# Kernel tuning notes

Measured on AMD Instinct MI355X. Metric: run time of the kernel, lower is better.

Reference implementation:

```python
import jax, jax.numpy as jnp
import numpy as np
from jax import lax

KERNEL = 3      # patch size
STRIDE = 1      # matching stride at low res
RATE = 2        # downsample rate
SOFTMAX_SCALE = 10.0


def _extract_patches(img, k, stride):
    """tf.image.extract_patches with SAME padding. img: [B,H,W,C] -> [B, oh*ow, k, k, C]."""
    B, H, W, C = img.shape
    oh = -(-H // stride)
    ow = -(-W // stride)
    ph = max((oh - 1) * stride + k - H, 0)
    pw = max((ow - 1) * stride + k - W, 0)
    img = jnp.pad(img, ((0, 0), (ph // 2, ph - ph // 2), (pw // 2, pw - pw // 2), (0, 0)))
    # stack the k*k shifted strided views; channel-last order matches TF's (kh, kw, C) flattening
    cols = [img[:, dh:dh + (oh - 1) * stride + 1:stride, dw:dw + (ow - 1) * stride + 1:stride, :]
            for dh in range(k) for dw in range(k)]
    p = jnp.stack(cols, axis=3)  # [B, oh, ow, k*k, C]
    return p.reshape(B, oh * ow, k, k, C)


def _avgpool2(x):
    """Exact equivalent of TF bilinear (antialias=False) downsample by factor 2."""
    B, H, W, C = x.shape
    return x.reshape(B, H // 2, 2, W // 2, 2, C).mean(axis=(2, 4))


def _conv_same(x4, w):
    return lax.conv_general_dilated(x4, w, (1, 1), 'SAME',
                                    dimension_numbers=('NHWC', 'HWIO', 'NHWC'))


def _forward(x, mask):
    B, H, W, C = x.shape
    k, stride, rate = KERNEL, STRIDE, RATE
    h, w = H // rate, W // rate
    L = h * w

    # raw (full-res) patches used for reconstruction: [B,k,k,C,L]
    raw_w = jnp.transpose(_extract_patches(x, k, rate * stride), (0, 2, 3, 4, 1))
    # low-res foreground / background (identical here, as in the source)
    f = _avgpool2(x)              # [B,h,w,C]
    m = _avgpool2(mask)           # [B,h,w,1]
    # low-res matching patches: [B,k,k,C,L]
    wp = jnp.transpose(_extract_patches(f, k, stride), (0, 2, 3, 4, 1))
    # mask patches -> gate: mm = 1 where the 3x3 mask patch mean is exactly 1.0
    mp = _extract_patches(m, k, stride)                       # [B,L,k,k,1]
    mm = (jnp.mean(mp, axis=(2, 3, 4)) == 1.0).astype(jnp.float32)  # [B,L]

    fuse_w = jnp.eye(KERNEL, dtype=jnp.float32).reshape(KERNEL, KERNEL, 1, 1)

    def per_item(xi, wi, rwi, mmi):
        # xi:[h,w,C]  wi,rwi:[k,k,C,L]  mmi:[L]
        wn = wi / jnp.maximum(jnp.sqrt(jnp.sum(wi * wi, axis=(0, 1, 2))), 1e-4)
        yi = _conv_same(xi[None], wn)          # [1,h,w,L] cosine-similarity logits
        att = yi[0]
        # fuse: diagonal conv over the [L,L] score matrix in both patch orderings
        z = yi.reshape(1, L, L, 1)
        z = _conv_same(z, fuse_w)
        z = z.reshape(1, h, w, h, w).transpose(0, 2, 1, 4, 3).reshape(1, L, L, 1)
        z = _conv_same(z, fuse_w)
        z = z.reshape(1, w, h, w, h).transpose(0, 2, 1, 4, 3)
        yi = z.reshape(1, h, w, L)
        mm4 = mmi.reshape(1, 1, 1, L)
        yi = jax.nn.softmax(yi * mm4 * SOFTMAX_SCALE, axis=3) * mm4
        # reconstruction: transposed conv with raw full-res patches as filters
        out = lax.conv_transpose(yi, rwi, (rate, rate), 'SAME',
                                 dimension_numbers=('NHWC', 'HWIO', 'NHWC'),
                                 transpose_kernel=True) / float(rate * rate)
        return out[0], att

    y, att = jax.vmap(per_item)(f, wp, raw_w, mm)
    return y, att


def setup_inputs() -> dict:
    key = jax.random.key(0)
    x = jax.random.normal(key, (2, 128, 128, 64), dtype=jnp.float32)
    # binary hole mask: ones inside a centered 64x64 square
    mask = jnp.zeros((2, 128, 128, 1), jnp.float32).at[:, 32:96, 32:96, :].set(1.0)
    return {"x": x, "mask": mask}


def reference(x, mask):
    return _forward(x, mask)
```

## Files before the change

### kernel.cpp

```cpp
#include <hip/hip_runtime.h>
#include <hip/hip_bf16.h>

typedef _Float16 f16x8 __attribute__((ext_vector_type(8)));
typedef float f32x4 __attribute__((ext_vector_type(4)));

__device__ __forceinline__ void gload_lds16(const void* gptr, void* lptr) {
  __builtin_amdgcn_global_load_lds(
      (const __attribute__((address_space(1))) void*)gptr,
      (__attribute__((address_space(3))) void*)lptr, 16, 0, 0);
}

__global__ __launch_bounds__(256) void k_pre(const float* __restrict__ x,
                                             const float* __restrict__ mask,
                                             _Float16* __restrict__ f_h,
                                             float* __restrict__ sumsq,
                                             float* __restrict__ mlow) {
  int wave = threadIdx.x >> 6, c = threadIdx.x & 63;
  int blk = blockIdx.x * 4 + wave;
  int b = blk >> 12, ij = blk & 4095;
  int i = ij >> 6, j = ij & 63;
  size_t base = ((size_t)(b * 128 + 2 * i) * 128 + 2 * j) * 64 + c;
  float f = 0.25f * (x[base] + x[base + 64] + x[base + 128 * 64] + x[base + 128 * 64 + 64]);
  f_h[(size_t)blk * 64 + c] = (_Float16)f;
  float fsq = f * f;
  for (int off = 32; off; off >>= 1) fsq += __shfl_down(fsq, off);
  if (c == 0) {
    sumsq[blk] = fsq;
    size_t mb = (size_t)(b * 128 + 2 * i) * 128 + 2 * j;
    mlow[blk] = 0.25f * (mask[mb] + mask[mb + 1] + mask[mb + 128] + mask[mb + 129]);
  }
}

__global__ void k_norm_mm(const float* __restrict__ sumsq, const float* __restrict__ mlow,
                          float* __restrict__ invn, float* __restrict__ mmb) {
  int t = blockIdx.x * 256 + threadIdx.x;
  int b = t >> 12, l = t & 4095;
  int li = l >> 6, lj = l & 63;
  float s = 0.f;
  bool ok = true;
  for (int dh = -1; dh <= 1; ++dh)
    for (int dw = -1; dw <= 1; ++dw) {
      int ii = li + dh, jj = lj + dw;
      float mv = 0.f;
      if ((unsigned)ii < 64u && (unsigned)jj < 64u) {
        int idx = (b << 12) + ii * 64 + jj;
        s += sumsq[idx];
        mv = mlow[idx];
      }
      ok = ok && (mv == 1.0f);
    }
  invn[t] = 1.0f / fmaxf(sqrtf(s), 1e-4f);
  mmb[t] = ok ? 1.0f : 0.0f;
}

__global__ __launch_bounds__(1024) void k_compact(const float* __restrict__ mmb,
                                                  int* __restrict__ actIdx,
                                                  int* __restrict__ nAct) {
  int b = blockIdx.x;
  int t = threadIdx.x;
  int lane = t & 63, wv = t >> 6;
  __shared__ int wsum[16];
  __shared__ int sbase;
  if (t == 0) sbase = 0;
  __syncthreads();
  for (int chunk = 0; chunk < 4; ++chunk) {
    int l = chunk * 1024 + t;
    int flag = (mmb[(b << 12) + l] == 1.0f) ? 1 : 0;
    unsigned long long m = __ballot(flag);
    int wpre = __popcll(m & ((1ull << lane) - 1ull));
    if (lane == 0) wsum[wv] = __popcll(m);
    __syncthreads();
    int off = sbase;
    for (int w2 = 0; w2 < wv; ++w2) off += wsum[w2];
    if (flag) {
      int pos = off + wpre;
      if (pos < 1024) actIdx[(b << 10) + pos] = l;
    }
    __syncthreads();
    if (t == 0) {
      int s2 = 0;
      for (int w2 = 0; w2 < 16; ++w2) s2 += wsum[w2];
      sbase += s2;
    }
    __syncthreads();
  }
  int total = sbase;
  if (t >= total) actIdx[(b << 10) + t] = 0;
  if (t == 0) nAct[b] = (total > 1024) ? 1024 : total;
}

__global__ __launch_bounds__(256) void k_build_p(const _Float16* __restrict__ f_h,
                                                 _Float16* __restrict__ P) {
  int wave = threadIdx.x >> 6, c = threadIdx.x & 63;
  int blk = blockIdx.x * 4 + wave;
  int b = blk >> 12, l = blk & 4095;
  int li = l >> 6, lj = l & 63;
  _Float16* dst = P + (size_t)blk * 576 + c;
#pragma unroll
  for (int kk = 0; kk < 9; ++kk) {
    int kh = kk / 3, kw = kk % 3;
    int ii = li + kh - 1, jj = lj + kw - 1;
    _Float16 v = (_Float16)0.f;
    if ((unsigned)ii < 64u && (unsigned)jj < 64u)
      v = f_h[((size_t)(b << 12) + ii * 64 + jj) * 64 + c];
    dst[kk * 64] = v;
  }
}

__global__ void k_build_rt(const float* __restrict__ x, _Float16* __restrict__ Rt) {
  int kh = blockIdx.x, li = blockIdx.y, b = blockIdx.z;
  int r = 2 * li + kh;
  __shared__ float xrow[128 * 65];
  if (r < 128) {
    for (int t = threadIdx.x; t < 8192; t += 256) {
      int v = t >> 6, c = t & 63;
      xrow[v * 65 + c] = x[((size_t)(b * 128 + r) * 128 + v) * 64 + c];
    }
  }
  __syncthreads();
  for (int idx = threadIdx.x; idx < 12288; idx += 256) {
    int lj = idx & 63, rest = idx >> 6;
    int c = rest & 63, kw = rest >> 6;
    int v = 2 * lj + kw;
    float val = (r < 128 && v < 128) ? xrow[v * 65 + c] : 0.f;
    int n = (kh * 3 + kw) * 64 + c;
    Rt[((size_t)b * 640 + n) * 4096 + li * 64 + lj] = (_Float16)val;
  }
}

__global__ void k_rtsub(const _Float16* __restrict__ Rt, const int* __restrict__ actIdx,
                        _Float16* __restrict__ Rts) {
  int n = blockIdx.x, b = blockIdx.y;
  const _Float16* src = Rt + ((size_t)b * 640 + n) * 4096;
  _Float16* dst = Rts + ((size_t)b * 640 + n) * 1024;
  const int* aIdx = actIdx + (b << 10);
  for (int s = threadIdx.x; s < 1024; s += 256) dst[s] = src[aIdx[s]];
}

__global__ __launch_bounds__(256) void k_gemm_sim(const _Float16* __restrict__ P,
                                                  const float* __restrict__ invn,
                                                  float* __restrict__ att) {
  int b = blockIdx.z;
  const _Float16* Ab = P + (size_t)b * 4096 * 576;
  int idx = blockIdx.x;
  int bj = (int)((sqrtf(8.f * (float)idx + 1.f) - 1.f) * 0.5f);
  while ((bj + 1) * (bj + 2) / 2 <= idx) ++bj;
  while (bj * (bj + 1) / 2 > idx) --bj;
  int bi = idx - bj * (bj + 1) / 2;
  int rowBase = bi * 128, colBase = bj * 128;
  bool diag = (bi == bj);

  __shared__ alignas(16) _Float16 As[128 * 32];
  __shared__ alignas(16) _Float16 Bs[128 * 32];
  __shared__ alignas(16) float tbuf[32][132];
  int tid = threadIdx.x, wave = tid >> 6, lane = tid & 63;
  int q = lane >> 4, rr = lane & 15;
  int wr = (wave >> 1) * 64, wc = (wave & 1) * 64;
  f32x4 acc[4][4] = {};
  for (int kt = 0; kt < 576; kt += 32) {
    __syncthreads();
#pragma unroll
    for (int t = 0; t < 2; ++t) {
      int chunk = t * 256 + wave * 64 + lane;
      int row = chunk >> 2, kc = (chunk & 3) * 8;
      gload_lds16(Ab + (size_t)(rowBase + row) * 576 + kt + kc,
                  As + (size_t)(t * 256 + wave * 64) * 8);
      if (!diag)
        gload_lds16(Ab + (size_t)(colBase + row) * 576 + kt + kc,
                    Bs + (size_t)(t * 256 + wave * 64) * 8);
    }
    __syncthreads();
    const _Float16* Bsrc = diag ? As : Bs;
    f16x8 af[4], bf[4];
#pragma unroll
    for (int mi = 0; mi < 4; ++mi)
      af[mi] = *(const f16x8*)(As + (wr + mi * 16 + rr) * 32 + q * 8);
#pragma unroll
    for (int ni = 0; ni < 4; ++ni)
      bf[ni] = *(const f16x8*)(Bsrc + (wc + ni * 16 + rr) * 32 + q * 8);
#pragma unroll
    for (int mi = 0; mi < 4; ++mi)
#pragma unroll
      for (int ni = 0; ni < 4; ++ni)
        acc[mi][ni] = __builtin_amdgcn_mfma_f32_16x16x32_f16(af[mi], bf[ni], acc[mi][ni], 0, 0, 0);
  }
  float* attb = att + ((size_t)b << 24);
#pragma unroll
  for (int ni = 0; ni < 4; ++ni) {
    int gc = colBase + wc + ni * 16 + rr;
    float sc = invn[(b << 12) + gc];
#pragma unroll
    for (int mi = 0; mi < 4; ++mi)
#pragma unroll
      for (int reg = 0; reg < 4; ++reg) {
        int gr = rowBase + wr + mi * 16 + q * 4 + reg;
        attb[((size_t)gr << 12) + gc] = acc[mi][ni][reg] * sc;
      }
  }
  if (diag) return;
  const float* ivrow = invn + (b << 12) + rowBase;
#pragma unroll
  for (int ph = 0; ph < 4; ++ph) {
    __syncthreads();
    if ((ph >> 1) == (wc >> 6)) {
      int nlo = (ph & 1) * 2;
#pragma unroll
      for (int nn = 0; nn < 2; ++nn) {
        int ni = nlo + nn;
        int rloc = nn * 16 + rr;
#pragma unroll
        for (int mi = 0; mi < 4; ++mi)
          *(f32x4*)&tbuf[rloc][wr + mi * 16 + q * 4] = acc[mi][ni];
      }
    }
    __syncthreads();
    int r = tid >> 3;
    int cbase = (tid & 7) * 16;
    int grow = colBase + ph * 32 + r;
    float* dst = attb + ((size_t)grow << 12) + rowBase + cbase;
#pragma unroll
    for (int cc = 0; cc < 16; cc += 4) {
      f32x4 v = *(f32x4*)&tbuf[r][cbase + cc];
      f32x4 s = *(const f32x4*)(ivrow + cbase + cc);
      *(f32x4*)(dst + cc) = v * s;
    }
  }
}

__global__ __launch_bounds__(256) void k_fuse_softmax3(const float* __restrict__ att,
                                                       const int* __restrict__ actIdx,
                                                       const int* __restrict__ nAct,
                                                       _Float16* __restrict__ Asub) {
  int blk0 = blockIdx.x;
  int blk = (blk0 & 7) * 1024 + (blk0 >> 3);
  int b = blk >> 12, p = blk & 4095;
  const float* Y = att + ((size_t)b << 24);
  const int* aIdx = actIdx + (b << 10);
  int na = nAct[b];
  int tid = threadIdx.x;
  int pi = p >> 6, pj = p & 63;
  int acol = pj * 64 + pi;

  int ls[4];
  bool act[4];
  float F[4] = {0.f, 0.f, 0.f, 0.f};
#pragma unroll
  for (int s4 = 0; s4 < 4; ++s4) {
    int slot = s4 * 256 + tid;
    ls[s4] = aIdx[slot];
    act[s4] = (slot < na);
  }

#pragma unroll
  for (int d2 = -1; d2 <= 1; ++d2) {
    int a2 = acol + d2;
    if ((unsigned)a2 >= 4096u) continue;
    int p2 = ((a2 & 63) << 6) | (a2 >> 6);
    int l2[4];
    bool lok[4];
#pragma unroll
    for (int s4 = 0; s4 < 4; ++s4) {
      int l = ls[s4];
      int bcol = ((l & 63) << 6) | (l >> 6);
      int b2 = bcol + d2;
      lok[s4] = act[s4] && ((unsigned)b2 < 4096u);
      int b2c = lok[s4] ? b2 : 0;
      l2[s4] = ((b2c & 63) << 6) | (b2c >> 6);
    }
#pragma unroll
    for (int d1 = -1; d1 <= 1; ++d1) {
      int qq = p2 + d1;
      if ((unsigned)qq >= 4096u) continue;
      const float* row = Y + ((size_t)qq << 12);
#pragma unroll
      for (int s4 = 0; s4 < 4; ++s4) {
        int rr2 = l2[s4] + d1;
        if (lok[s4] && (unsigned)rr2 < 4096u) F[s4] += row[rr2];
      }
    }
  }

  float z[4];
  float mx = (na < 4096) ? 0.f : -1e30f;
#pragma unroll
  for (int s4 = 0; s4 < 4; ++s4) {
    z[s4] = act[s4] ? F[s4] * 10.f : -1e30f;
    mx = fmaxf(mx, z[s4]);
  }
  __shared__ float red[4];
  for (int off = 32; off; off >>= 1) mx = fmaxf(mx, __shfl_down(mx, off));
  if ((tid & 63) == 0) red[tid >> 6] = mx;
  __syncthreads();
  mx = fmaxf(fmaxf(red[0], red[1]), fmaxf(red[2], red[3]));
  float e[4];
  float esum = 0.f;
#pragma unroll
  for (int s4 = 0; s4 < 4; ++s4) {
    e[s4] = act[s4] ? __expf(z[s4] - mx) : 0.f;
    esum += e[s4];
  }
  for (int off = 32; off; off >>= 1) esum += __shfl_down(esum, off);
  __syncthreads();
  if ((tid & 63) == 0) red[tid >> 6] = esum;
  __syncthreads();
  float total = red[0] + red[1] + red[2] + red[3] + (float)(4096 - na) * __expf(0.f - mx);
  float inv = 1.f / total;
  _Float16* Ap = Asub + ((size_t)blk << 10);
#pragma unroll
  for (int s4 = 0; s4 < 4; ++s4) Ap[s4 * 256 + tid] = (_Float16)(e[s4] * inv);
}

__global__ __launch_bounds__(256) void k_gemm_recon(const _Float16* __restrict__ Asub,
                                                    const _Float16* __restrict__ Rts,
                                                    float* __restrict__ y) {
  int b = blockIdx.z;
  const _Float16* Ab = Asub + ((size_t)b << 22);
  const _Float16* Bb = Rts + (size_t)b * 640 * 1024;
  int rowBase = blockIdx.y * 128, colBase = blockIdx.x * 128;
  __shared__ alignas(16) _Float16 As[128 * 32];
  __shared__ alignas(16) _Float16 Bs[128 * 32];
  int tid = threadIdx.x, wave = tid >> 6, lane = tid & 63;
  int q = lane >> 4, rr = lane & 15;
  int wr = (wave >> 1) * 64, wc = (wave & 1) * 64;
  f32x4 acc[4][4] = {};
  for (int kt = 0; kt < 1024; kt += 32) {
    __syncthreads();
#pragma unroll
    for (int t = 0; t < 2; ++t) {
      int chunk = t * 256 + wave * 64 + lane;
      int row = chunk >> 2, kc = (chunk & 3) * 8;
      gload_lds16(Ab + ((size_t)(rowBase + row) << 10) + kt + kc,
                  As + (size_t)(t * 256 + wave * 64) * 8);
      gload_lds16(Bb + ((size_t)(colBase + row) << 10) + kt + kc,
                  Bs + (size_t)(t * 256 + wave * 64) * 8);
    }
    __syncthreads();
    f16x8 af[4], bf[4];
#pragma unroll
    for (int mi = 0; mi < 4; ++mi)
      af[mi] = *(const f16x8*)(As + (wr + mi * 16 + rr) * 32 + q * 8);
#pragma unroll
    for (int ni = 0; ni < 4; ++ni)
      bf[ni] = *(const f16x8*)(Bs + (wc + ni * 16 + rr) * 32 + q * 8);
#pragma unroll
    for (int mi = 0; mi < 4; ++mi)
#pragma unroll
      for (int ni = 0; ni < 4; ++ni)
        acc[mi][ni] = __builtin_amdgcn_mfma_f32_16x16x32_f16(af[mi], bf[ni], acc[mi][ni], 0, 0, 0);
  }
#pragma unroll
  for (int ni = 0; ni < 4; ++ni) {
    int gc = colBase + wc + ni * 16 + rr;
    if (gc < 576) {
      int kk = gc >> 6, c = gc & 63;
      int kh = kk / 3, kw = kk - kh * 3;
#pragma unroll
      for (int mi = 0; mi < 4; ++mi)
#pragma unroll
        for (int reg = 0; reg < 4; ++reg) {
          int gp = rowBase + wr + mi * 16 + q * 4 + reg;
          int i = gp >> 6, j = gp & 63;
          int u = 2 * i + kh, v = 2 * j + kw;
          if (u < 128 && v < 128)
            atomicAdd(y + (((size_t)((b * 128 + u) * 128 + v)) << 6) + c,
                      0.25f * acc[mi][ni][reg]);
        }
    }
  }
}

extern "C" void kernel_launch(void* const* d_in, const int* in_sizes, int n_in,
                              void* d_out, int out_size, void* d_ws, size_t ws_size,
                              hipStream_t stream) {
  const float* x = (const float*)d_in[0];
  const float* mask = (const float*)d_in[1];
  float* out = (float*)d_out;
  float* y = out;
  float* att = out + 2097152;

  char* ws = (char*)d_ws;
  _Float16* f_h = (_Float16*)(ws + 0);
  float* sumsq = (float*)(ws + 0x100000);
  float* mlow = (float*)(ws + 0x108000);
  float* invn = (float*)(ws + 0x110000);
  float* mmb = (float*)(ws + 0x118000);
  _Float16* P = (_Float16*)(ws + 0x120000);
  _Float16* Rt = (_Float16*)(ws + 0xA20000);
  int* actIdx = (int*)(ws + 0x1420000);
  int* nAct = (int*)(ws + 0x1422000);
  _Float16* Rts = (_Float16*)(ws + 0x1430000);
  _Float16* Asub = (_Float16*)(ws + 0x16B0000);
  (void)in_sizes; (void)n_in; (void)out_size; (void)ws_size;

  hipMemsetAsync(y, 0, (size_t)2097152 * 4, stream);

  k_pre<<<2048, 256, 0, stream>>>(x, mask, f_h, sumsq, mlow);
  k_norm_mm<<<32, 256, 0, stream>>>(sumsq, mlow, invn, mmb);
  k_compact<<<2, 1024, 0, stream>>>(mmb, actIdx, nAct);
  k_build_p<<<2048, 256, 0, stream>>>(f_h, P);
  k_build_rt<<<dim3(3, 64, 2), 256, 0, stream>>>(x, Rt);
  k_rtsub<<<dim3(640, 2), 256, 0, stream>>>(Rt, actIdx, Rts);
  k_gemm_sim<<<dim3(528, 1, 2), 256, 0, stream>>>(P, invn, att);
  k_fuse_softmax3<<<8192, 256, 0, stream>>>(att, actIdx, nAct, Asub);
  k_gemm_recon<<<dim3(5, 32, 2), 256, 0, stream>>>(Asub, Rts, y);
}
```

Measured before the change: 302.9 us.

## Double GEMM K-tile to 64 with XOR-swizzled LDS and fuse norm/compact kernels

Both MFMA GEMMs (similarity and reconstruction) now stage 64-wide K tiles in LDS instead of 32. This halves the number of barrier-separated load phases, and an XOR swizzle on the 16-byte chunk index avoids LDS bank conflicts on the fragment reads. Separately, the norm/mask kernel and the compaction kernel are merged into one launch that keeps the mask flags in shared memory, removing a kernel launch and the mmb global round trip. The cost is that the fused prologue now runs on only 2 blocks, and LDS use per GEMM block doubles, which may reduce occupancy.

```diff
diff --git a/kernel.cpp b/kernel.cpp
--- a/kernel.cpp
+++ b/kernel.cpp
@@ -31,33 +31,33 @@
   }
 }
 
-__global__ void k_norm_mm(const float* __restrict__ sumsq, const float* __restrict__ mlow,
-                          float* __restrict__ invn, float* __restrict__ mmb) {
-  int t = blockIdx.x * 256 + threadIdx.x;
-  int b = t >> 12, l = t & 4095;
-  int li = l >> 6, lj = l & 63;
-  float s = 0.f;
-  bool ok = true;
-  for (int dh = -1; dh <= 1; ++dh)
-    for (int dw = -1; dw <= 1; ++dw) {
-      int ii = li + dh, jj = lj + dw;
-      float mv = 0.f;
-      if ((unsigned)ii < 64u && (unsigned)jj < 64u) {
-        int idx = (b << 12) + ii * 64 + jj;
-        s += sumsq[idx];
-        mv = mlow[idx];
-      }
-      ok = ok && (mv == 1.0f);
-    }
-  invn[t] = 1.0f / fmaxf(sqrtf(s), 1e-4f);
-  mmb[t] = ok ? 1.0f : 0.0f;
-}
-
-__global__ __launch_bounds__(1024) void k_compact(const float* __restrict__ mmb,
-                                                  int* __restrict__ actIdx,
-                                                  int* __restrict__ nAct) {
+__global__ __launch_bounds__(1024) void k_norm_compact(const float* __restrict__ sumsq,
+                                                       const float* __restrict__ mlow,
+                                                       float* __restrict__ invn,
+                                                       int* __restrict__ actIdx,
+                                                       int* __restrict__ nAct) {
   int b = blockIdx.x;
   int t = threadIdx.x;
+  __shared__ unsigned char mmf[4096];
+  for (int l = t; l < 4096; l += 1024) {
+    int li = l >> 6, lj = l & 63;
+    float s = 0.f;
+    bool ok = true;
+    for (int dh = -1; dh <= 1; ++dh)
+      for (int dw = -1; dw <= 1; ++dw) {
+        int ii = li + dh, jj = lj + dw;
+        float mv = 0.f;
+        if ((unsigned)ii < 64u && (unsigned)jj < 64u) {
+          int idx = (b << 12) + ii * 64 + jj;
+          s += sumsq[idx];
+          mv = mlow[idx];
+        }
+        ok = ok && (mv == 1.0f);
+      }
+    invn[(b << 12) + l] = 1.0f / fmaxf(sqrtf(s), 1e-4f);
+    mmf[l] = ok ? 1 : 0;
+  }
+  __syncthreads();
   int lane = t & 63, wv = t >> 6;
   __shared__ int wsum[16];
   __shared__ int sbase;
@@ -65,7 +65,7 @@
   __syncthreads();
   for (int chunk = 0; chunk < 4; ++chunk) {
     int l = chunk * 1024 + t;
-    int flag = (mmb[(b << 12) + l] == 1.0f) ? 1 : 0;
+    int flag = mmf[l] ? 1 : 0;
     unsigned long long m = __ballot(flag);
     int wpre = __popcll(m & ((1ull << lane) - 1ull));
     if (lane == 0) wsum[wv] = __popcll(m);
@@ -150,19 +150,20 @@
   int rowBase = bi * 128, colBase = bj * 128;
   bool diag = (bi == bj);
 
-  __shared__ alignas(16) _Float16 As[128 * 32];
-  __shared__ alignas(16) _Float16 Bs[128 * 32];
+  __shared__ alignas(16) _Float16 As[128 * 64];
+  __shared__ alignas(16) _Float16 Bs[128 * 64];
   __shared__ alignas(16) float tbuf[32][132];
   int tid = threadIdx.x, wave = tid >> 6, lane = tid & 63;
   int q = lane >> 4, rr = lane & 15;
   int wr = (wave >> 1) * 64, wc = (wave & 1) * 64;
   f32x4 acc[4][4] = {};
-  for (int kt = 0; kt < 576; kt += 32) {
-    __syncthreads();
-#pragma unroll
-    for (int t = 0; t < 2; ++t) {
+  for (int kt = 0; kt < 576; kt += 64) {
+    __syncthreads();
+#pragma unroll
+    for (int t = 0; t < 4; ++t) {
       int chunk = t * 256 + wave * 64 + lane;
-      int row = chunk >> 2, kc = (chunk & 3) * 8;
+      int row = chunk >> 3;
+      int kc = ((chunk & 7) ^ (row & 7)) * 8;
       gload_lds16(Ab + (size_t)(rowBase + row) * 576 + kt + kc,
                   As + (size_t)(t * 256 + wave * 64) * 8);
       if (!diag)
@@ -171,18 +172,27 @@
     }
     __syncthreads();
     const _Float16* Bsrc = diag ? As : Bs;
-    f16x8 af[4], bf[4];
-#pragma unroll
-    for (int mi = 0; mi < 4; ++mi)
-      af[mi] = *(const f16x8*)(As + (wr + mi * 16 + rr) * 32 + q * 8);
-#pragma unroll
-    for (int ni = 0; ni < 4; ++ni)
-      bf[ni] = *(const f16x8*)(Bsrc + (wc + ni * 16 + rr) * 32 + q * 8);
-#pragma unroll
-    for (int mi = 0; mi < 4; ++mi)
-#pragma unroll
-      for (int ni = 0; ni < 4; ++ni)
-        acc[mi][ni] = __builtin_amdgcn_mfma_f32_16x16x32_f16(af[mi], bf[ni], acc[mi][ni], 0, 0, 0);
+#pragma unroll
+    for (int ks = 0; ks < 2; ++ks) {
+      f16x8 af[4], bf[4];
+#pragma unroll
+      for (int mi = 0; mi < 4; ++mi) {
+        int r = wr + mi * 16 + rr;
+        int ps = (ks * 4 + q) ^ (r & 7);
+        af[mi] = *(const f16x8*)(As + r * 64 + ps * 8);
+      }
+#pragma unroll
+      for (int ni = 0; ni < 4; ++ni) {
+        int r = wc + ni * 16 + rr;
+        int ps = (ks * 4 + q) ^ (r & 7);
+        bf[ni] = *(const f16x8*)(Bsrc + r * 64 + ps * 8);
+      }
+#pragma unroll
+      for (int mi = 0; mi < 4; ++mi)
+#pragma unroll
+        for (int ni = 0; ni < 4; ++ni)
+          acc[mi][ni] = __builtin_amdgcn_mfma_f32_16x16x32_f16(af[mi], bf[ni], acc[mi][ni], 0, 0, 0);
+    }
   }
   float* attb = att + ((size_t)b << 24);
 #pragma unroll
@@ -317,36 +327,46 @@
   const _Float16* Ab = Asub + ((size_t)b << 22);
   const _Float16* Bb = Rts + (size_t)b * 640 * 1024;
   int rowBase = blockIdx.y * 128, colBase = blockIdx.x * 128;
-  __shared__ alignas(16) _Float16 As[128 * 32];
-  __shared__ alignas(16) _Float16 Bs[128 * 32];
+  __shared__ alignas(16) _Float16 As[128 * 64];
+  __shared__ alignas(16) _Float16 Bs[128 * 64];
   int tid = threadIdx.x, wave = tid >> 6, lane = tid & 63;
   int q = lane >> 4, rr = lane & 15;
   int wr = (wave >> 1) * 64, wc = (wave & 1) * 64;
   f32x4 acc[4][4] = {};
-  for (int kt = 0; kt < 1024; kt += 32) {
-    __syncthreads();
-#pragma unroll
-    for (int t = 0; t < 2; ++t) {
+  for (int kt = 0; kt < 1024; kt += 64) {
+    __syncthreads();
+#pragma unroll
+    for (int t = 0; t < 4; ++t) {
       int chunk = t * 256 + wave * 64 + lane;
-      int row = chunk >> 2, kc = (chunk & 3) * 8;
+      int row = chunk >> 3;
+      int kc = ((chunk & 7) ^ (row & 7)) * 8;
       gload_lds16(Ab + ((size_t)(rowBase + row) << 10) + kt + kc,
                   As + (size_t)(t * 256 + wave * 64) * 8);
       gload_lds16(Bb + ((size_t)(colBase + row) << 10) + kt + kc,
                   Bs + (size_t)(t * 256 + wave * 64) * 8);
     }
     __syncthreads();
-    f16x8 af[4], bf[4];
-#pragma unroll
-    for (int mi = 0; mi < 4; ++mi)
-      af[mi] = *(const f16x8*)(As + (wr + mi * 16 + rr) * 32 + q * 8);
-#pragma unroll
-    for (int ni = 0; ni < 4; ++ni)
-      bf[ni] = *(const f16x8*)(Bs + (wc + ni * 16 + rr) * 32 + q * 8);
-#pragma unroll
-    for (int mi = 0; mi < 4; ++mi)
-#pragma unroll
-      for (int ni = 0; ni < 4; ++ni)
-        acc[mi][ni] = __builtin_amdgcn_mfma_f32_16x16x32_f16(af[mi], bf[ni], acc[mi][ni], 0, 0, 0);
+#pragma unroll
+    for (int ks = 0; ks < 2; ++ks) {
+      f16x8 af[4], bf[4];
+#pragma unroll
+      for (int mi = 0; mi < 4; ++mi) {
+        int r = wr + mi * 16 + rr;
+        int ps = (ks * 4 + q) ^ (r & 7);
+        af[mi] = *(const f16x8*)(As + r * 64 + ps * 8);
+      }
+#pragma unroll
+      for (int ni = 0; ni < 4; ++ni) {
+        int r = wc + ni * 16 + rr;
+        int ps = (ks * 4 + q) ^ (r & 7);
+        bf[ni] = *(const f16x8*)(Bs + r * 64 + ps * 8);
+      }
+#pragma unroll
+      for (int mi = 0; mi < 4; ++mi)
+#pragma unroll
+        for (int ni = 0; ni < 4; ++ni)
+          acc[mi][ni] = __builtin_amdgcn_mfma_f32_16x16x32_f16(af[mi], bf[ni], acc[mi][ni], 0, 0, 0);
+    }
   }
 #pragma unroll
   for (int ni = 0; ni < 4; ++ni) {
@@ -383,7 +403,6 @@
   float* sumsq = (float*)(ws + 0x100000);
   float* mlow = (float*)(ws + 0x108000);
   float* invn = (float*)(ws + 0x110000);
-  float* mmb = (float*)(ws + 0x118000);
   _Float16* P = (_Float16*)(ws + 0x120000);
   _Float16* Rt = (_Float16*)(ws + 0xA20000);
   int* actIdx = (int*)(ws + 0x1420000);
@@ -395,8 +414,7 @@
   hipMemsetAsync(y, 0, (size_t)2097152 * 4, stream);
 
   k_pre<<<2048, 256, 0, stream>>>(x, mask, f_h, sumsq, mlow);
-  k_norm_mm<<<32, 256, 0, stream>>>(sumsq, mlow, invn, mmb);
-  k_compact<<<2, 1024, 0, stream>>>(mmb, actIdx, nAct);
+  k_norm_compact<<<2, 1024, 0, stream>>>(sumsq, mlow, invn, actIdx, nAct);
   k_build_p<<<2048, 256, 0, stream>>>(f_h, P);
   k_build_rt<<<dim3(3, 64, 2), 256, 0, stream>>>(x, Rt);
   k_rtsub<<<dim3(640, 2), 256, 0, stream>>>(Rt, actIdx, Rts);
```

Result: faster. 295.2 us (-2.5%).
